# Optimization experiments

Measured on AMD Instinct MI355X. Metric: run time of the kernel, lower is better.

Reference implementation:

```python
import jax, jax.numpy as jnp
import numpy as np

B, T, C, H, W = 4, 5, 512, 32, 32   # bt = B*T = 20
G = 32                              # GroupNorm groups
EPS = 1e-6


def group_norm(x, gamma, beta):
    # x: [N, C, H, W]; normalize per (group-channels, H, W)
    n, c, h, w = x.shape
    xg = x.reshape(n, G, c // G, h * w)
    mu = jnp.mean(xg, axis=(2, 3), keepdims=True)
    var = jnp.mean((xg - mu) ** 2, axis=(2, 3), keepdims=True)
    xn = ((xg - mu) * jax.lax.rsqrt(var + EPS)).reshape(n, c, h, w)
    return xn * gamma[None, :, None, None] + beta[None, :, None, None]


def conv1x1(x, w, b):
    # 1x1 conv == channel matmul. x: [N,C,H,W], w: [O,C], b: [O]
    return jnp.einsum('nchw,oc->nohw', x, w) + b[None, :, None, None]


def setup_inputs() -> dict:
    key = jax.random.key(0)
    ks = jax.random.split(key, 9)
    inp = {'x': jax.random.normal(ks[0], (B * T, C, H, W), jnp.float32)}
    for i, nm in enumerate(['wq', 'wk', 'wv', 'wo', 'wqt', 'wkt', 'wvt', 'wot']):
        inp[nm] = jax.random.normal(ks[i + 1], (C, C), jnp.float32) * 0.02
        inp['b' + nm[1:]] = jnp.zeros((C,), jnp.float32)
    inp['gamma_s'] = jnp.ones((C,), jnp.float32)
    inp['beta_s'] = jnp.zeros((C,), jnp.float32)
    inp['gamma_t'] = jnp.ones((C,), jnp.float32)
    inp['beta_t'] = jnp.zeros((C,), jnp.float32)
    return inp


def reference(x, wq, bq, wk, bk, wv, bv, wo, bo,
              wqt, bqt, wkt, bkt, wvt, bvt, wot, bot,
              gamma_s, beta_s, gamma_t, beta_t):
    scale = float(C) ** -0.5

    # ---- spatial attention (AttnBlock.forward) ----
    hn = group_norm(x, gamma_s, beta_s)
    q = conv1x1(hn, wq, bq).reshape(B * T, C, H * W)
    k = conv1x1(hn, wk, bk).reshape(B * T, C, H * W)
    v = conv1x1(hn, wv, bv).reshape(B * T, C, H * W)
    # scores [bt, hw_q, hw_k], softmax over keys
    att = jax.nn.softmax(jnp.einsum('bcq,bck->bqk', q, k) * scale, axis=2)
    hsp = jnp.einsum('bck,bqk->bcq', v, att).reshape(B * T, C, H, W)
    spatio = x + conv1x1(hsp, wo, bo)

    # ---- temporal attention across t=5 frames per pixel ----
    hn = group_norm(spatio, gamma_t, beta_t)
    q5 = conv1x1(hn, wqt, bqt).reshape(B, T, C, H, W)
    k5 = conv1x1(hn, wkt, bkt).reshape(B, T, C, H, W)
    v5 = conv1x1(hn, wvt, bvt).reshape(B, T, C, H, W)
    # per-pixel [t, t] attention, softmax over key-frame axis s
    att_t = jax.nn.softmax(jnp.einsum('btchw,bschw->bhwts', q5, k5) * scale, axis=-1)
    htp = jnp.einsum('bhwts,bschw->btchw', att_t, v5).reshape(B * T, C, H, W)

    # NOTE: residual is the ORIGINAL x (faithful to the source), not spatio
    return x + conv1x1(htp, wot, bot)
```

## Files before the change

kernel.cpp:

```cpp
#include <hip/hip_runtime.h>
#include <hip/hip_bf16.h>
#include <stdint.h>

typedef unsigned short u16;
typedef __attribute__((ext_vector_type(8))) short bf16x8;
typedef __attribute__((ext_vector_type(4))) float f32x4;

#define DI __device__ __forceinline__

DI float b2f(u16 u) { return __uint_as_float(((uint32_t)u) << 16); }
DI u16 f2b(float f) {
  uint32_t u = __float_as_uint(f);
  u += 0x7fff + ((u >> 16) & 1);
  return (u16)(u >> 16);
}

DI void gld_lds16(const u16* g, u16* l) {
  __builtin_amdgcn_global_load_lds((const __attribute__((address_space(1))) void*)g,
                                   (__attribute__((address_space(3))) void*)l,
                                   16, 0, 0);
}

__global__ __launch_bounds__(256)
void setup_wb(const float* __restrict__ w0, const float* __restrict__ w1,
              const float* __restrict__ w2, const float* __restrict__ w3,
              const float* __restrict__ w4, const float* __restrict__ w5,
              const float* __restrict__ w6, const float* __restrict__ w7,
              const float* __restrict__ b0, const float* __restrict__ b1,
              const float* __restrict__ b2, const float* __restrict__ b3,
              const float* __restrict__ b4, const float* __restrict__ b5,
              const float* __restrict__ b6, const float* __restrict__ b7,
              u16* __restrict__ dst, float* __restrict__ bdst)
{
  if (blockIdx.x >= 1024) {
    const float* bs[8] = {b0, b1, b2, b3, b4, b5, b6, b7};
    const int a = blockIdx.x - 1024;
    const int i = threadIdx.x;
    bdst[a * 512 + i] = bs[a][i];
    bdst[a * 512 + i + 256] = bs[a][i + 256];
    return;
  }
  const float* srcs[8] = {w0, w1, w2, w3, w4, w5, w6, w7};
  const int mat = blockIdx.x >> 7;
  const int i = (((blockIdx.x & 127) << 8) + threadIdx.x) * 8;
  const float* s = srcs[mat];
  float4 a = *(const float4*)(s + i);
  float4 b = *(const float4*)(s + i + 4);
  alignas(16) u16 v[8] = {f2b(a.x), f2b(a.y), f2b(a.z), f2b(a.w),
                          f2b(b.x), f2b(b.y), f2b(b.z), f2b(b.w)};
  *(uint4*)(dst + (long)mat * 262144 + i) = *(const uint4*)v;
}

template<int OUTF32, int BIASMODE, int RESID>
__global__ __launch_bounds__(256)
void gemm_bt(const u16* __restrict__ A, long sA, long lda,
             const u16* __restrict__ B, long sB, long ldb,
             void* __restrict__ C, long sC,
             const float* __restrict__ bias,
             const float* __restrict__ resid, long sR,
             int N, int K, float alpha)
{
  __shared__ u16 lA[2 * 128 * 32];
  __shared__ u16 lB[2 * 128 * 32];
  const int t = threadIdx.x;
  const int lane = t & 63;
  const int wid = t >> 6;

  const int nx = gridDim.x;
  const int bid = blockIdx.y * nx + blockIdx.x;
  const int nper = (nx * gridDim.y) >> 3;
  const int nid = (bid & 7) * nper + (bid >> 3);
  const int m0 = (nid / nx) * 128, n0 = (nid % nx) * 128;

  const long bz = blockIdx.z;
  const u16* Ab = A + bz * sA;
  const u16* Bb = B + bz * sB;

  const int row = t >> 2;
  const int kc  = (((t & 3) ^ ((t >> 3) & 3)) << 3);

  f32x4 acc[4][4];
#pragma unroll
  for (int i = 0; i < 4; ++i)
#pragma unroll
    for (int j = 0; j < 4; ++j) acc[i][j] = (f32x4){0.f, 0.f, 0.f, 0.f};

  const int ml = lane & 15, qd = lane >> 4;
  const int koff = ((qd ^ ((ml >> 1) & 3)) << 3);
  const int wm = (wid >> 1) * 64, wn = (wid & 1) * 64;

  auto stage = [&](int bsel, int k0) {
    const u16* Ap = Ab + (long)(m0 + row) * lda + (k0 + kc);
    const u16* Bp = Bb + (long)(n0 + row) * ldb + (k0 + kc);
    u16* la = lA + bsel * 4096 + wid * 512;
    u16* lb = lB + bsel * 4096 + wid * 512;
    gld_lds16(Ap, la);
    gld_lds16(Ap + 64 * lda, la + 2048);
    gld_lds16(Bp, lb);
    gld_lds16(Bp + 64 * ldb, lb + 2048);
  };

  const int niter = K >> 5;
  stage(0, 0);
  for (int i = 0; i < niter; ++i) {
    __syncthreads();
    if (i + 1 < niter) stage((i + 1) & 1, (i + 1) << 5);
    const u16* la = lA + (i & 1) * 4096;
    const u16* lb = lB + (i & 1) * 4096;
    bf16x8 af[4], bfr[4];
#pragma unroll
    for (int x = 0; x < 4; ++x)
      af[x] = *(const bf16x8*)&la[(wm + x * 16 + ml) * 32 + koff];
#pragma unroll
    for (int y = 0; y < 4; ++y)
      bfr[y] = *(const bf16x8*)&lb[(wn + y * 16 + ml) * 32 + koff];
#pragma unroll
    for (int x = 0; x < 4; ++x)
#pragma unroll
      for (int y = 0; y < 4; ++y)
        acc[x][y] = __builtin_amdgcn_mfma_f32_16x16x32_bf16(af[x], bfr[y], acc[x][y], 0, 0, 0);
  }

  const long cb = bz * sC;
#pragma unroll
  for (int i = 0; i < 4; ++i) {
#pragma unroll
    for (int j = 0; j < 4; ++j) {
#pragma unroll
      for (int r = 0; r < 4; ++r) {
        int rr = m0 + wm + i * 16 + qd * 4 + r;
        int cc = n0 + wn + j * 16 + ml;
        float v = acc[i][j][r] * alpha;
        if (BIASMODE == 1) v += bias[rr];
        if (BIASMODE == 2) v += bias[cc];
        long idx = (long)rr * N + cc;
        if (RESID) v += resid[bz * sR + idx];
        if (OUTF32) ((float*)C)[cb + idx] = v;
        else        ((u16*)C)[cb + idx] = f2b(v);
      }
    }
  }
}

__global__ __launch_bounds__(256)
void groupnorm_f32(const float* __restrict__ x, const float* __restrict__ gamma,
                   const float* __restrict__ beta, u16* __restrict__ out)
{
  const int C = 512, HW = 1024;
  const int n = blockIdx.x >> 5, g = blockIdx.x & 31;
  const float* xg = x + ((long)n * C + g * 16) * HW;
  const int t = threadIdx.x;
  float s = 0.f, ss = 0.f;
  for (int ch = t; ch < 4096; ch += 256) {
    float4 u = *(const float4*)(xg + ch * 4);
    s += u.x + u.y + u.z + u.w;
    ss += u.x * u.x + u.y * u.y + u.z * u.z + u.w * u.w;
  }
#pragma unroll
  for (int off = 32; off > 0; off >>= 1) { s += __shfl_xor(s, off); ss += __shfl_xor(ss, off); }
  __shared__ float rs[4], rss[4];
  if ((t & 63) == 0) { rs[t >> 6] = s; rss[t >> 6] = ss; }
  __syncthreads();
  s  = rs[0] + rs[1] + rs[2] + rs[3];
  ss = rss[0] + rss[1] + rss[2] + rss[3];
  const float mu = s * (1.f / 16384.f);
  const float var = ss * (1.f / 16384.f) - mu * mu;
  const float rstd = rsqrtf(var + 1e-6f);
  float gm[16], bt[16];
#pragma unroll
  for (int i = 0; i < 16; ++i) {
    float ga = gamma[g * 16 + i];
    gm[i] = ga * rstd;
    bt[i] = beta[g * 16 + i] - mu * ga * rstd;
  }
  for (int p = t; p < 1024; p += 256) {
    alignas(16) u16 vals[16];
#pragma unroll
    for (int i = 0; i < 16; ++i)
      vals[i] = f2b(xg[(long)i * HW + p] * gm[i] + bt[i]);
    u16* dst = out + ((long)n * HW + p) * C + g * 16;
    *(uint4*)dst       = *(const uint4*)&vals[0];
    *(uint4*)(dst + 8) = *(const uint4*)&vals[8];
  }
}

__global__ __launch_bounds__(256)
void groupnorm_bf16(const u16* __restrict__ x, const float* __restrict__ gamma,
                    const float* __restrict__ beta, u16* __restrict__ out)
{
  const int C = 512, HW = 1024;
  const int n = blockIdx.x >> 5, g = blockIdx.x & 31;
  const u16* xg = x + ((long)n * C + g * 16) * HW;
  const int t = threadIdx.x;
  float s = 0.f, ss = 0.f;
  for (int ch = t; ch < 2048; ch += 256) {
    uint4 u = *(const uint4*)(xg + ch * 8);
    uint32_t w[4] = {u.x, u.y, u.z, u.w};
#pragma unroll
    for (int k = 0; k < 4; ++k) {
      float f0 = __uint_as_float(w[k] << 16);
      float f1 = __uint_as_float(w[k] & 0xffff0000u);
      s += f0 + f1; ss += f0 * f0 + f1 * f1;
    }
  }
#pragma unroll
  for (int off = 32; off > 0; off >>= 1) { s += __shfl_xor(s, off); ss += __shfl_xor(ss, off); }
  __shared__ float rs[4], rss[4];
  if ((t & 63) == 0) { rs[t >> 6] = s; rss[t >> 6] = ss; }
  __syncthreads();
  s  = rs[0] + rs[1] + rs[2] + rs[3];
  ss = rss[0] + rss[1] + rss[2] + rss[3];
  const float mu = s * (1.f / 16384.f);
  const float var = ss * (1.f / 16384.f) - mu * mu;
  const float rstd = rsqrtf(var + 1e-6f);
  float gm[16], bt[16];
#pragma unroll
  for (int i = 0; i < 16; ++i) {
    float ga = gamma[g * 16 + i];
    gm[i] = ga * rstd;
    bt[i] = beta[g * 16 + i] - mu * ga * rstd;
  }
  for (int p = t; p < 1024; p += 256) {
    alignas(16) u16 vals[16];
#pragma unroll
    for (int i = 0; i < 16; ++i)
      vals[i] = f2b(b2f(xg[(long)i * HW + p]) * gm[i] + bt[i]);
    u16* dst = out + ((long)n * HW + p) * C + g * 16;
    *(uint4*)dst       = *(const uint4*)&vals[0];
    *(uint4*)(dst + 8) = *(const uint4*)&vals[8];
  }
}

__global__ __launch_bounds__(256)
void softmax1024(u16* __restrict__ data)
{
  u16* row = data + (long)blockIdx.x * 1024;
  const int t = threadIdx.x;
  uint2 u = *(const uint2*)(row + t * 4);
  float v[4];
  v[0] = __uint_as_float(u.x << 16); v[1] = __uint_as_float(u.x & 0xffff0000u);
  v[2] = __uint_as_float(u.y << 16); v[3] = __uint_as_float(u.y & 0xffff0000u);
  float mx = fmaxf(fmaxf(v[0], v[1]), fmaxf(v[2], v[3]));
#pragma unroll
  for (int off = 32; off > 0; off >>= 1) mx = fmaxf(mx, __shfl_xor(mx, off));
  __shared__ float red[8];
  if ((t & 63) == 0) red[t >> 6] = mx;
  __syncthreads();
  mx = fmaxf(fmaxf(red[0], red[1]), fmaxf(red[2], red[3]));
  float e[4]; float s = 0.f;
#pragma unroll
  for (int k = 0; k < 4; ++k) { e[k] = __expf(v[k] - mx); s += e[k]; }
#pragma unroll
  for (int off = 32; off > 0; off >>= 1) s += __shfl_xor(s, off);
  if ((t & 63) == 0) red[4 + (t >> 6)] = s;
  __syncthreads();
  s = red[4] + red[5] + red[6] + red[7];
  float inv = 1.f / s;
  uint2 o;
  o.x = (uint32_t)f2b(e[0] * inv) | ((uint32_t)f2b(e[1] * inv) << 16);
  o.y = (uint32_t)f2b(e[2] * inv) | ((uint32_t)f2b(e[3] * inv) << 16);
  *(uint2*)(row + t * 4) = o;
}

__global__ __launch_bounds__(256)
void temporal_attn(const u16* __restrict__ qkv, u16* __restrict__ htp)
{
  const int t = threadIdx.x;
  const int wv = t >> 6, lane = t & 63;
  const int pix = blockIdx.x * 4 + wv;
  const int b = pix >> 10, p = pix & 1023;
  const long fs = 1024l * 1536;
  const long rowbase = ((long)b * 5 * 1024 + p) * 1536 + lane * 8;

  float qf[5][8], kf[5][8];
#pragma unroll
  for (int f = 0; f < 5; ++f) {
    bf16x8 qv = *(const bf16x8*)(qkv + rowbase + f * fs);
    bf16x8 kv = *(const bf16x8*)(qkv + rowbase + f * fs + 512);
#pragma unroll
    for (int u = 0; u < 8; ++u) { qf[f][u] = b2f((u16)qv[u]); kf[f][u] = b2f((u16)kv[u]); }
  }
  float sc[25];
#pragma unroll
  for (int i = 0; i < 5; ++i)
#pragma unroll
    for (int j = 0; j < 5; ++j) {
      float a = 0.f;
#pragma unroll
      for (int u = 0; u < 8; ++u) a += qf[i][u] * kf[j][u];
      sc[i * 5 + j] = a;
    }
#pragma unroll
  for (int m = 1; m < 64; m <<= 1)
#pragma unroll
    for (int s = 0; s < 25; ++s) sc[s] += __shfl_xor(sc[s], m);

  const float scale = 0.04419417382415922f;
  float att[5][5];
#pragma unroll
  for (int i = 0; i < 5; ++i) {
    float m = sc[i * 5];
#pragma unroll
    for (int j = 1; j < 5; ++j) m = fmaxf(m, sc[i * 5 + j]);
    float ssum = 0.f;
#pragma unroll
    for (int j = 0; j < 5; ++j) { att[i][j] = __expf((sc[i * 5 + j] - m) * scale); ssum += att[i][j]; }
    float inv = 1.f / ssum;
#pragma unroll
    for (int j = 0; j < 5; ++j) att[i][j] *= inv;
  }

  float of[5][8];
#pragma unroll
  for (int i = 0; i < 5; ++i)
#pragma unroll
    for (int u = 0; u < 8; ++u) of[i][u] = 0.f;
#pragma unroll
  for (int s = 0; s < 5; ++s) {
    bf16x8 vvv = *(const bf16x8*)(qkv + rowbase + s * fs + 1024);
#pragma unroll
    for (int u = 0; u < 8; ++u) {
      float vf = b2f((u16)vvv[u]);
#pragma unroll
      for (int i = 0; i < 5; ++i) of[i][u] += att[i][s] * vf;
    }
  }
  const long obase = ((long)b * 5 * 1024 + p) * 512 + lane * 8;
#pragma unroll
  for (int i = 0; i < 5; ++i) {
    alignas(16) u16 ob[8];
#pragma unroll
    for (int u = 0; u < 8; ++u) ob[u] = f2b(of[i][u]);
    *(uint4*)(htp + obase + i * 1024 * 512) = *(const uint4*)ob;
  }
}

extern "C" void kernel_launch(void* const* d_in, const int* in_sizes, int n_in,
                              void* d_out, int out_size, void* d_ws, size_t ws_size,
                              hipStream_t stream)
{
  const float* x   = (const float*)d_in[0];
  const float* wq  = (const float*)d_in[1];
  const float* bq  = (const float*)d_in[2];
  const float* wk  = (const float*)d_in[3];
  const float* bk  = (const float*)d_in[4];
  const float* wv  = (const float*)d_in[5];
  const float* bv  = (const float*)d_in[6];
  const float* wo  = (const float*)d_in[7];
  const float* bo  = (const float*)d_in[8];
  const float* wqt = (const float*)d_in[9];
  const float* bqt = (const float*)d_in[10];
  const float* wkt = (const float*)d_in[11];
  const float* bkt = (const float*)d_in[12];
  const float* wvt = (const float*)d_in[13];
  const float* bvt = (const float*)d_in[14];
  const float* wot = (const float*)d_in[15];
  const float* bot = (const float*)d_in[16];
  const float* gs  = (const float*)d_in[17];
  const float* bs  = (const float*)d_in[18];
  const float* gt  = (const float*)d_in[19];
  const float* btt = (const float*)d_in[20];

  const long U = 20l * 1024 * 512;
  u16* W0 = (u16*)d_ws;
  u16* W1 = W0 + U;
  u16* W3 = W0 + 3 * U;
  u16* W4 = W0 + 4 * U;
  u16* W6 = W0 + 6 * U;
  u16* W7 = W0 + 7 * U;
  u16* Wt = W0 + 8 * U;
  float* Bf = (float*)(Wt + 8 * 262144);
  u16* wv_b  = Wt + 2 * 262144;
  u16* wo_b  = Wt + 3 * 262144;
  u16* wqt_b = Wt + 4 * 262144;
  u16* wot_b = Wt + 7 * 262144;

  const long S  = 524288;
  const long S2 = 1048576;
  const float scale = 0.04419417382415922f;
  dim3 blk(256);

  setup_wb<<<1032, blk, 0, stream>>>(wq, wk, wv, wo, wqt, wkt, wvt, wot,
                                     bq, bk, bv, bo, bqt, bkt, bvt, bot, Wt, Bf);

  groupnorm_f32<<<640, blk, 0, stream>>>(x, gs, bs, W0);
  gemm_bt<0, 2, 0><<<dim3(8, 160, 1), blk, 0, stream>>>(
      W0, 0, 512, Wt, 0, 512, W1, 0, Bf, nullptr, 0, 1024, 512, 1.f);
  gemm_bt<0, 1, 0><<<dim3(8, 4, 20), blk, 0, stream>>>(
      wv_b, 0, 512, W0, S, 512, W3, S, Bf + 1024, nullptr, 0, 1024, 512, 1.f);
  gemm_bt<0, 0, 0><<<dim3(8, 8, 20), blk, 0, stream>>>(
      W1, S2, 1024, W1 + 512, S2, 1024, W4, S2, nullptr, nullptr, 0, 1024, 512, scale);
  softmax1024<<<20480, blk, 0, stream>>>(W4);
  gemm_bt<0, 0, 0><<<dim3(4, 8, 20), blk, 0, stream>>>(
      W4, S2, 1024, W3, S, 1024, W0, S, nullptr, nullptr, 0, 512, 1024, 1.f);
  gemm_bt<0, 1, 1><<<dim3(8, 4, 20), blk, 0, stream>>>(
      wo_b, 0, 512, W0, S, 512, W6, S, Bf + 1536, x, S, 1024, 512, 1.f);
  groupnorm_bf16<<<640, blk, 0, stream>>>(W6, gt, btt, W7);
  gemm_bt<0, 2, 0><<<dim3(12, 160, 1), blk, 0, stream>>>(
      W7, 0, 512, wqt_b, 0, 512, W1, 0, Bf + 2048, nullptr, 0, 1536, 512, 1.f);
  temporal_attn<<<1024, blk, 0, stream>>>(W1, W0);
  gemm_bt<1, 1, 1><<<dim3(8, 4, 20), blk, 0, stream>>>(
      wot_b, 0, 512, W0, S, 512, (float*)d_out, S, Bf + 3584, x, S, 1024, 512, 1.f);
}
```

Measured before the change: 444.9 us.

## Replace 128x128 GEMM with 256x256-tile, 512-thread, 4-stage pipelined kernel

Swaps the double-buffered 128x128 bf16 MFMA GEMM for a 256x256 tile computed by 8 waves, each wave owning a 128x64 sub-tile. It uses a 4-deep global-to-LDS prefetch ring with explicit vmcnt waits and raw barriers, and raises scheduling priority around the MFMA bursts. The aim is more data reuse per LDS load and better hiding of load latency. In exchange, the XOR LDS swizzle is dropped, which may cause bank conflicts on reads. LDS use grows to 128KB per block, and several launches now have only 160 blocks, which can leave CUs idle.

```diff
diff --git a/kernel.cpp b/kernel.cpp
--- a/kernel.cpp
+++ b/kernel.cpp
@@ -52,85 +52,111 @@
 }
 
 template<int OUTF32, int BIASMODE, int RESID>
-__global__ __launch_bounds__(256)
-void gemm_bt(const u16* __restrict__ A, long sA, long lda,
+__global__ __launch_bounds__(512, 2)
+void gemm256(const u16* __restrict__ A, long sA, long lda,
              const u16* __restrict__ B, long sB, long ldb,
              void* __restrict__ C, long sC,
              const float* __restrict__ bias,
              const float* __restrict__ resid, long sR,
              int N, int K, float alpha)
 {
-  __shared__ u16 lA[2 * 128 * 32];
-  __shared__ u16 lB[2 * 128 * 32];
+  __shared__ u16 lA[32768];
+  __shared__ u16 lB[32768];
   const int t = threadIdx.x;
-  const int lane = t & 63;
-  const int wid = t >> 6;
+  const int lane = t & 63, wid = t >> 6;
+  const int wr = wid >> 2, wc = wid & 3;
+  const int ml = lane & 15, qd = lane >> 4;
 
   const int nx = gridDim.x;
   const int bid = blockIdx.y * nx + blockIdx.x;
   const int nper = (nx * gridDim.y) >> 3;
   const int nid = (bid & 7) * nper + (bid >> 3);
-  const int m0 = (nid / nx) * 128, n0 = (nid % nx) * 128;
+  const int m0 = (nid / nx) * 256, n0 = (nid % nx) * 256;
 
   const long bz = blockIdx.z;
   const u16* Ab = A + bz * sA;
   const u16* Bb = B + bz * sB;
 
-  const int row = t >> 2;
-  const int kc  = (((t & 3) ^ ((t >> 3) & 3)) << 3);
-
-  f32x4 acc[4][4];
-#pragma unroll
-  for (int i = 0; i < 4; ++i)
+  const int srow = t >> 2;
+  const int scol = (t & 3) << 3;
+  const u16* Ap0 = Ab + (long)(m0 + srow) * lda + scol;
+  const u16* Bp0 = Bb + (long)(n0 + srow) * ldb + scol;
+  u16* lwA = lA + (wid << 9);
+  u16* lwB = lB + (wid << 9);
+
+  f32x4 acc[8][4];
+#pragma unroll
+  for (int i = 0; i < 8; ++i)
 #pragma unroll
     for (int j = 0; j < 4; ++j) acc[i][j] = (f32x4){0.f, 0.f, 0.f, 0.f};
 
-  const int ml = lane & 15, qd = lane >> 4;
-  const int koff = ((qd ^ ((ml >> 1) & 3)) << 3);
-  const int wm = (wid >> 1) * 64, wn = (wid & 1) * 64;
-
-  auto stage = [&](int bsel, int k0) {
-    const u16* Ap = Ab + (long)(m0 + row) * lda + (k0 + kc);
-    const u16* Bp = Bb + (long)(n0 + row) * ldb + (k0 + kc);
-    u16* la = lA + bsel * 4096 + wid * 512;
-    u16* lb = lB + bsel * 4096 + wid * 512;
-    gld_lds16(Ap, la);
-    gld_lds16(Ap + 64 * lda, la + 2048);
-    gld_lds16(Bp, lb);
-    gld_lds16(Bp + 64 * ldb, lb + 2048);
+  const int NT = K >> 5;
+
+  auto stage = [&](int tk) {
+    const int boff = (tk & 3) << 13;
+    const u16* Ap = Ap0 + (tk << 5);
+    const u16* Bp = Bp0 + (tk << 5);
+    gld_lds16(Ap,             lwA + boff);
+    gld_lds16(Ap + lda * 128, lwA + boff + 4096);
+    gld_lds16(Bp,             lwB + boff);
+    gld_lds16(Bp + ldb * 128, lwB + boff + 4096);
   };
 
-  const int niter = K >> 5;
-  stage(0, 0);
-  for (int i = 0; i < niter; ++i) {
-    __syncthreads();
-    if (i + 1 < niter) stage((i + 1) & 1, (i + 1) << 5);
-    const u16* la = lA + (i & 1) * 4096;
-    const u16* lb = lB + (i & 1) * 4096;
-    bf16x8 af[4], bfr[4];
-#pragma unroll
-    for (int x = 0; x < 4; ++x)
-      af[x] = *(const bf16x8*)&la[(wm + x * 16 + ml) * 32 + koff];
-#pragma unroll
-    for (int y = 0; y < 4; ++y)
-      bfr[y] = *(const bf16x8*)&lb[(wn + y * 16 + ml) * 32 + koff];
-#pragma unroll
-    for (int x = 0; x < 4; ++x)
-#pragma unroll
-      for (int y = 0; y < 4; ++y)
-        acc[x][y] = __builtin_amdgcn_mfma_f32_16x16x32_bf16(af[x], bfr[y], acc[x][y], 0, 0, 0);
+  stage(0); stage(1); stage(2);
+  asm volatile("s_waitcnt vmcnt(8)" ::: "memory");
+  __builtin_amdgcn_s_barrier();
+  __builtin_amdgcn_sched_barrier(0);
+
+  const u16* rA = lA + (wr << 12) + ml * 32 + qd * 8;
+  const u16* rB = lB + (wc << 11) + ml * 32 + qd * 8;
+
+  for (int tk = 0; tk < NT; ++tk) {
+    if (tk + 3 < NT) stage(tk + 3);
+    const int boff = (tk & 3) << 13;
+    const u16* pa = rA + boff;
+    const u16* pb = rB + boff;
+    bf16x8 bfr[4], af[4];
+#pragma unroll
+    for (int n = 0; n < 4; ++n) bfr[n] = *(const bf16x8*)(pb + n * 512);
+#pragma unroll
+    for (int m = 0; m < 4; ++m) af[m] = *(const bf16x8*)(pa + m * 512);
+    __builtin_amdgcn_s_setprio(1);
+#pragma unroll
+    for (int m = 0; m < 4; ++m)
+#pragma unroll
+      for (int n = 0; n < 4; ++n)
+        acc[m][n] = __builtin_amdgcn_mfma_f32_16x16x32_bf16(af[m], bfr[n], acc[m][n], 0, 0, 0);
+    __builtin_amdgcn_s_setprio(0);
+#pragma unroll
+    for (int m = 0; m < 4; ++m) af[m] = *(const bf16x8*)(pa + (m + 4) * 512);
+    __builtin_amdgcn_s_setprio(1);
+#pragma unroll
+    for (int m = 0; m < 4; ++m)
+#pragma unroll
+      for (int n = 0; n < 4; ++n)
+        acc[m + 4][n] = __builtin_amdgcn_mfma_f32_16x16x32_bf16(af[m], bfr[n], acc[m + 4][n], 0, 0, 0);
+    __builtin_amdgcn_s_setprio(0);
+
+    if (tk < NT - 1) {
+      const int rem = NT - 2 - tk;
+      if (rem >= 2)      asm volatile("s_waitcnt vmcnt(8)" ::: "memory");
+      else if (rem == 1) asm volatile("s_waitcnt vmcnt(4)" ::: "memory");
+      else               asm volatile("s_waitcnt vmcnt(0)" ::: "memory");
+      __builtin_amdgcn_s_barrier();
+      __builtin_amdgcn_sched_barrier(0);
+    }
   }
 
   const long cb = bz * sC;
 #pragma unroll
-  for (int i = 0; i < 4; ++i) {
-#pragma unroll
-    for (int j = 0; j < 4; ++j) {
+  for (int mt = 0; mt < 8; ++mt) {
+#pragma unroll
+    for (int nt = 0; nt < 4; ++nt) {
 #pragma unroll
       for (int r = 0; r < 4; ++r) {
-        int rr = m0 + wm + i * 16 + qd * 4 + r;
-        int cc = n0 + wn + j * 16 + ml;
-        float v = acc[i][j][r] * alpha;
+        int rr = m0 + wr * 128 + mt * 16 + qd * 4 + r;
+        int cc = n0 + wc * 64 + nt * 16 + ml;
+        float v = acc[mt][nt][r] * alpha;
         if (BIASMODE == 1) v += bias[rr];
         if (BIASMODE == 2) v += bias[cc];
         long idx = (long)rr * N + cc;
@@ -379,26 +405,27 @@
   const long S2 = 1048576;
   const float scale = 0.04419417382415922f;
   dim3 blk(256);
+  dim3 blk5(512);
 
   setup_wb<<<1032, blk, 0, stream>>>(wq, wk, wv, wo, wqt, wkt, wvt, wot,
                                      bq, bk, bv, bo, bqt, bkt, bvt, bot, Wt, Bf);
 
   groupnorm_f32<<<640, blk, 0, stream>>>(x, gs, bs, W0);
-  gemm_bt<0, 2, 0><<<dim3(8, 160, 1), blk, 0, stream>>>(
+  gemm256<0, 2, 0><<<dim3(4, 80, 1), blk5, 0, stream>>>(
       W0, 0, 512, Wt, 0, 512, W1, 0, Bf, nullptr, 0, 1024, 512, 1.f);
-  gemm_bt<0, 1, 0><<<dim3(8, 4, 20), blk, 0, stream>>>(
+  gemm256<0, 1, 0><<<dim3(4, 2, 20), blk5, 0, stream>>>(
       wv_b, 0, 512, W0, S, 512, W3, S, Bf + 1024, nullptr, 0, 1024, 512, 1.f);
-  gemm_bt<0, 0, 0><<<dim3(8, 8, 20), blk, 0, stream>>>(
+  gemm256<0, 0, 0><<<dim3(4, 4, 20), blk5, 0, stream>>>(
       W1, S2, 1024, W1 + 512, S2, 1024, W4, S2, nullptr, nullptr, 0, 1024, 512, scale);
   softmax1024<<<20480, blk, 0, stream>>>(W4);
-  gemm_bt<0, 0, 0><<<dim3(4, 8, 20), blk, 0, stream>>>(
+  gemm256<0, 0, 0><<<dim3(2, 4, 20), blk5, 0, stream>>>(
       W4, S2, 1024, W3, S, 1024, W0, S, nullptr, nullptr, 0, 512, 1024, 1.f);
-  gemm_bt<0, 1, 1><<<dim3(8, 4, 20), blk, 0, stream>>>(
+  gemm256<0, 1, 1><<<dim3(4, 2, 20), blk5, 0, stream>>>(
       wo_b, 0, 512, W0, S, 512, W6, S, Bf + 1536, x, S, 1024, 512, 1.f);
   groupnorm_bf16<<<640, blk, 0, stream>>>(W6, gt, btt, W7);
-  gemm_bt<0, 2, 0><<<dim3(12, 160, 1), blk, 0, stream>>>(
+  gemm256<0, 2, 0><<<dim3(6, 80, 1), blk5, 0, stream>>>(
       W7, 0, 512, wqt_b, 0, 512, W1, 0, Bf + 2048, nullptr, 0, 1536, 512, 1.f);
   temporal_attn<<<1024, blk, 0, stream>>>(W1, W0);
-  gemm_bt<1, 1, 1><<<dim3(8, 4, 20), blk, 0, stream>>>(
+  gemm256<1, 1, 1><<<dim3(4, 2, 20), blk5, 0, stream>>>(
       wot_b, 0, 512, W0, S, 512, (float*)d_out, S, Bf + 3584, x, S, 1024, 512, 1.f);
 }
```

Result: slower. 496.1 us (+11.5%).
